# Performance work log

Measured on AMD Instinct MI355X. Metric: run time of the kernel, lower is better.

## Reference

```python
import jax, jax.numpy as jnp
import numpy as np

K = 20  # max object ids (ids 1..K); masks value 0 = background
EPS_GN = 1e-5

def _conv3(x, w, b):
    # 3x3 conv, padding=1 == SAME, NCHW/OIHW
    y = jax.lax.conv_general_dilated(x, w, (1, 1), 'SAME',
                                     dimension_numbers=('NCHW', 'OIHW', 'NCHW'))
    return y + b[None, :, None, None]

def _groupnorm(x, groups, w, b):
    B, C, H, W = x.shape
    xg = x.reshape(B, groups, C // groups, H, W)
    m = xg.mean(axis=(2, 3, 4), keepdims=True)
    v = xg.var(axis=(2, 3, 4), keepdims=True)
    xn = ((xg - m) * jax.lax.rsqrt(v + EPS_GN)).reshape(B, C, H, W)
    return xn * w[None, :, None, None] + b[None, :, None, None]


def setup_inputs() -> dict:
    key = jax.random.key(0)
    ks = jax.random.split(key, 8)
    def p(k, shape, s=0.05):
        return jax.random.normal(k, shape, jnp.float32) * s
    return {
        'x': jax.random.normal(ks[0], (4, 512, 128, 128), jnp.float32),
        'masks': jax.random.randint(ks[1], (4, 128, 128), 0, 21, jnp.int32),
        'w1': p(ks[2], (256, 512, 3, 3)), 'b1': jnp.zeros((256,), jnp.float32),
        'g1w': jnp.ones((256,), jnp.float32), 'g1b': jnp.zeros((256,), jnp.float32),
        'w2': p(ks[3], (128, 256, 3, 3)), 'b2': jnp.zeros((128,), jnp.float32),
        'g2w': jnp.ones((128,), jnp.float32), 'g2b': jnp.zeros((128,), jnp.float32),
        'w3': p(ks[4], (64, 128, 3, 3)), 'b3': jnp.zeros((64,), jnp.float32),
        'g3w': jnp.ones((64,), jnp.float32), 'g3b': jnp.zeros((64,), jnp.float32),
        'wb': p(ks[5], (7, 64)), 'bb': jnp.zeros((7,), jnp.float32),
        'wc': p(ks[6], (1, 64)), 'bc': jnp.zeros((1,), jnp.float32),
    }


def reference(x, masks, w1, b1, g1w, g1b, w2, b2, g2w, g2b,
              w3, b3, g3w, g3b, wb, bb, wc, bc):
    # encoder: (conv3 -> GN -> relu) x3
    h = jax.nn.relu(_groupnorm(_conv3(x, w1, b1), 8, g1w, g1b))
    h = jax.nn.relu(_groupnorm(_conv3(h, w2, b2), 4, g2w, g2b))
    h = jax.nn.relu(_groupnorm(_conv3(h, w3, b3), 4, g3w, g3b))  # [B,64,H,W]

    # masked segment-mean pooling over all ids 1..K (vectorized unique-loop)
    ids = jnp.arange(1, K + 1, dtype=masks.dtype)
    onehot = (masks[:, None, :, :] == ids[None, :, None, None]).astype(h.dtype)  # [B,K,H,W]
    sums = jnp.einsum('bchw,bkhw->bkc', h, onehot)          # [B,K,64]
    counts = onehot.sum(axis=(2, 3))                        # [B,K]
    pooled = sums / (counts[..., None] + 1e-6)              # [B,K,64]

    # 1x1 conv heads on pooled vector == dense matmuls
    boxes = jnp.einsum('bkc,oc->bko', pooled, wb) + bb      # [B,K,7]
    scores = jax.nn.sigmoid(jnp.einsum('bkc,oc->bko', pooled, wc) + bc)[..., 0]  # [B,K]
    return (boxes, scores)
```

## Files before the change

### kernel.cpp

```cpp
#include <hip/hip_runtime.h>
#include <hip/hip_bf16.h>
#include <math.h>

#define HW 16384
#define BATCH 4
#define KIDS 20

using short8 = __attribute__((ext_vector_type(8))) short;
using f32x4  = __attribute__((ext_vector_type(4))) float;

__device__ __forceinline__ unsigned short bfbits(float f) {
  __hip_bfloat16 h = __float2bfloat16(f);
  return *(unsigned short*)&h;
}

__device__ __forceinline__ void gload_lds16(const void* g, void* l) {
  __builtin_amdgcn_global_load_lds(
      (const __attribute__((address_space(1))) void*)g,
      (__attribute__((address_space(3))) void*)l, 16, 0, 0);
}

__global__ __launch_bounds__(256) void zero_k(float* __restrict__ p, int n) {
  int i = blockIdx.x*256 + threadIdx.x;
  if (i < n) p[i] = 0.f;
}

__global__ __launch_bounds__(256) void x_to_nhwc_k(const float* __restrict__ in,
                                                   __hip_bfloat16* __restrict__ out)
{
  __shared__ float tile[32][65];
  int t = blockIdx.x;
  const int pxt = t & 255; t >>= 8;
  const int ct  = t & 15;  t >>= 4;
  const int b   = t;
  const int tid = threadIdx.x;
  #pragma unroll
  for (int it = 0; it < 8; ++it) {
    int idx = tid + it*256;
    int px_l = idx & 63, c_l = idx >> 6;
    tile[c_l][px_l] = in[((size_t)(b*512 + ct*32 + c_l))*HW + pxt*64 + px_l];
  }
  __syncthreads();
  #pragma unroll
  for (int it = 0; it < 4; ++it) {
    int idx = tid + it*256;
    int c2 = idx & 15, px_l = idx >> 4;
    unsigned u = ((unsigned)bfbits(tile[c2*2+1][px_l]) << 16) | bfbits(tile[c2*2][px_l]);
    *(unsigned*)(out + ((size_t)(b*HW + pxt*64 + px_l))*512 + ct*32 + c2*2) = u;
  }
}

template<int Co, int Ci>
__global__ __launch_bounds__(256) void pack_w_k(const float* __restrict__ w,
                                                __hip_bfloat16* __restrict__ out)
{
  const int i = blockIdx.x*256 + threadIdx.x;
  const int ci = i & (Ci-1);
  const int r  = i >> __builtin_ctz(Ci);
  const int co = r & (Co-1);
  const int t  = r >> __builtin_ctz(Co);
  out[i] = __float2bfloat16(w[((size_t)co*Ci + ci)*9 + t]);
}

template<int Ci, int Co, int CPG, int MT>
__global__ __launch_bounds__(512, 2) void conv_mfma_k(
    const __hip_bfloat16* __restrict__ xin,
    const __hip_bfloat16* __restrict__ wpk,
    const float* __restrict__ bias,
    float* __restrict__ out,
    float* __restrict__ partS, float* __restrict__ partSS)
{
  constexpr int NT  = 4;
  constexpr int RG  = 64;
  constexpr int NC  = Ci/32;
  constexpr int NGW = (MT*16)/CPG;
  constexpr int WCO = 2*MT*16;
  constexpr int WSEG = WCO/16;
  constexpr int IBs = 4*10*512;
  constexpr int WLs = 9*WSEG*512;
  __shared__ __align__(16) short lds[2*IBs + WLs + 512];
  short* const wlds  = lds + 2*IBs;
  short* const trash = lds + 2*IBs + WLs;

  const int b  = blockIdx.x / RG;
  const int r0 = (blockIdx.x % RG) * 2;
  const int co0 = blockIdx.y * WCO;
  const int tid = threadIdx.x;
  const int wave = tid >> 6, lane = tid & 63;
  const int row_w = wave & 1;
  const int pw    = (wave >> 1) & 1;
  const int coh   = wave >> 2;
  const int co_w  = co0 + coh*MT*16;
  const int y = r0 + row_w;
  const int lr = lane & 15, q = lane >> 4;
  const int ls = lane & 15, lq = lane >> 4;

  {
    short8 z = {0,0,0,0,0,0,0,0};
    for (int i = tid; i < 1024; i += 512) {
      int u = i >> 6, m = i & 63;
      int buf = u >> 3, r = (u >> 1) & 3, side = u & 1;
      *((short8*)(lds + buf*IBs + r*5120 + side*9*512) + m) = z;
    }
    if (r0 == 0) {
      for (int i = tid; i < 2*640; i += 512) {
        int buf = i / 640, m = i % 640;
        *((short8*)(lds + buf*IBs + 0*5120) + m) = z;
      }
    }
    if (r0 == 126) {
      for (int i = tid; i < 2*640; i += 512) {
        int buf = i / 640, m = i % 640;
        *((short8*)(lds + buf*IBs + 3*5120) + m) = z;
      }
    }
  }

  const size_t in_base = (size_t)b * HW * Ci;

  auto stage_i = [&](int buf, int ci0) {
    #pragma unroll
    for (int it = 0; it < 4; ++it) {
      int gi = wave*4 + it;
      int r = gi >> 3, sd = (gi & 7) + 1;
      int yy = r0 + r - 1;
      bool ok = (unsigned)yy < 128u;
      int yc = ok ? yy : 0;
      const __hip_bfloat16* src = xin + in_base
          + (size_t)(yc*128 + (sd-1)*16 + ls)*Ci + ci0 + lq*8;
      short* dst = ok ? (lds + buf*IBs + r*5120 + sd*512) : trash;
      gload_lds16(src, dst);
    }
  };
  auto stage_w = [&](int ci0) {
    for (int u = wave; u < 9*WSEG; u += 8) {
      int t = u / WSEG, cs = u % WSEG;
      gload_lds16(wpk + ((size_t)(t*Co + co0 + cs*16 + ls))*Ci + ci0 + lq*8,
                  wlds + u*512);
    }
  };

  int base_dx[3];
  #pragma unroll
  for (int dx = 0; dx < 3; ++dx) {
    int e = dx + 15 + lr;
    base_dx[dx] = row_w*5120 + pw*2048 + (e>>4)*512 + (e&15)*8 + q*128;
  }
  const int base_a = coh*MT*512 + q*128 + lr*8;

  f32x4 acc[MT][NT] = {};
  stage_i(0, 0);
  __syncthreads();
  int cur = 0;
  for (int c = 0; c < NC; ++c) {
    const int ci0 = c*32;
    stage_w(ci0);
    if (c+1 < NC) {
      stage_i(cur^1, ci0 + 32);
      asm volatile("s_waitcnt vmcnt(4)" ::: "memory");
    } else {
      asm volatile("s_waitcnt vmcnt(0)" ::: "memory");
    }
    __builtin_amdgcn_s_barrier();
    __builtin_amdgcn_sched_barrier(0);
    const short* ib = lds + cur*IBs;

    short8 af[2][MT], bf[2][NT];
    #pragma unroll
    for (int mt = 0; mt < MT; ++mt)
      af[0][mt] = *(const short8*)(wlds + base_a + mt*512);
    #pragma unroll
    for (int nt = 0; nt < NT; ++nt)
      bf[0][nt] = *(const short8*)(ib + base_dx[0] + nt*512);

    #pragma unroll
    for (int t = 0; t < 9; ++t) {
      const int cb = t & 1, nb = cb ^ 1;
      if (t < 8) {
        const int t1 = t + 1, dy1 = t1/3, dx1 = t1%3;
        const short* wt = wlds + t1*WSEG*512;
        #pragma unroll
        for (int mt = 0; mt < MT; ++mt)
          af[nb][mt] = *(const short8*)(wt + base_a + mt*512);
        #pragma unroll
        for (int nt = 0; nt < NT; ++nt)
          bf[nb][nt] = *(const short8*)(ib + base_dx[dx1] + dy1*5120 + nt*512);
      }
      #pragma unroll
      for (int mt = 0; mt < MT; ++mt)
        #pragma unroll
        for (int nt = 0; nt < NT; ++nt)
          acc[mt][nt] = __builtin_amdgcn_mfma_f32_16x16x32_bf16(
              af[cb][mt], bf[cb][nt], acc[mt][nt], 0, 0, 0);
    }
    __builtin_amdgcn_s_barrier();
    cur ^= 1;
  }

  float sg[NGW] = {}, ssg[NGW] = {};
  #pragma unroll
  for (int mt = 0; mt < MT; ++mt) {
    const int g = (mt*16) / CPG;
    #pragma unroll
    for (int nt = 0; nt < NT; ++nt) {
      int px = pw*64 + nt*16 + lr;
      int co = co_w + mt*16 + q*4;
      const float4 bv = *(const float4*)(bias + co);
      f32x4 v = acc[mt][nt];
      v[0] += bv.x; v[1] += bv.y; v[2] += bv.z; v[3] += bv.w;
      sg[g]  += v[0] + v[1] + v[2] + v[3];
      ssg[g] += v[0]*v[0] + v[1]*v[1] + v[2]*v[2] + v[3]*v[3];
      *(f32x4*)(out + ((size_t)(b*HW + y*128 + px))*Co + co) = v;
    }
  }
  const int bgbase = b*(Co/CPG) + co_w/CPG;
  #pragma unroll
  for (int g = 0; g < NGW; ++g) {
    float s = sg[g], ss = ssg[g];
    #pragma unroll
    for (int off = 32; off; off >>= 1) {
      s  += __shfl_xor(s, off);
      ss += __shfl_xor(ss, off);
    }
    if (lane == 0) {
      atomicAdd(&partS[bgbase + g], s);
      atomicAdd(&partSS[bgbase + g], ss);
    }
  }
}

__global__ void gn_final_k(const float* __restrict__ partS,
                           const float* __restrict__ partSS,
                           float* __restrict__ mv, int nbg, float inv_n)
{
  const int i = threadIdx.x;
  if (i < nbg) {
    float s = partS[i], ss = partSS[i];
    float mean = s*inv_n, var = ss*inv_n - mean*mean;
    mv[2*i] = mean; mv[2*i+1] = rsqrtf(var + 1e-5f);
  }
}

template<int C, int CPG, bool BF16OUT>
__global__ __launch_bounds__(256) void gn_apply_k(const float* __restrict__ in,
    const float* __restrict__ mv, const float* __restrict__ gw,
    const float* __restrict__ gb, void* __restrict__ outp)
{
  constexpr int C4 = C/4;
  constexpr int G = C/CPG;
  const int i = blockIdx.x*256 + threadIdx.x;
  const int c4 = i & (C4-1);
  const int pxb = i >> __builtin_ctz(C4);
  const int b = pxb >> 14;
  const int c = c4*4;
  const int bg = b*G + c/CPG;
  const float mean = mv[2*bg], inv = mv[2*bg+1];
  float4 v = *((const float4*)in + i);
  const float4 w4 = *(const float4*)(gw + c);
  const float4 b4 = *(const float4*)(gb + c);
  float r0 = fmaxf((v.x-mean)*inv*w4.x + b4.x, 0.f);
  float r1 = fmaxf((v.y-mean)*inv*w4.y + b4.y, 0.f);
  float r2 = fmaxf((v.z-mean)*inv*w4.z + b4.z, 0.f);
  float r3 = fmaxf((v.w-mean)*inv*w4.w + b4.w, 0.f);
  if (BF16OUT) {
    uint2 o;
    o.x = ((unsigned)bfbits(r1) << 16) | bfbits(r0);
    o.y = ((unsigned)bfbits(r3) << 16) | bfbits(r2);
    *(uint2*)((__hip_bfloat16*)outp + (size_t)i*4) = o;
  } else {
    *((float4*)outp + i) = make_float4(r0,r1,r2,r3);
  }
}

__global__ __launch_bounds__(256) void pool_counts_k(
    const int* __restrict__ masks, float* __restrict__ counts)
{
  __shared__ int hist[KIDS];
  const int b = blockIdx.x;
  if (threadIdx.x < KIDS) hist[threadIdx.x] = 0;
  __syncthreads();
  for (int p = threadIdx.x; p < HW; p += 256) {
    const int m = masks[b*HW + p];
    if (m > 0) atomicAdd(&hist[m-1], 1);
  }
  __syncthreads();
  if (threadIdx.x < KIDS) counts[b*KIDS + threadIdx.x] = (float)hist[threadIdx.x];
}

__global__ __launch_bounds__(256) void pool_sums_k(const float* __restrict__ h3,
    const int* __restrict__ masks, float* __restrict__ sums)
{
  __shared__ float acc[KIDS*64];
  const int b = blockIdx.x >> 5, chunk = blockIdx.x & 31;
  const int tid = threadIdx.x;
  for (int j = tid; j < KIDS*64; j += 256) acc[j] = 0.f;
  __syncthreads();
  const int ch = tid & 63, pi = tid >> 6;
  const int p0 = chunk*512;
  for (int p = p0 + pi; p < p0 + 512; p += 4) {
    int m = masks[b*HW + p];
    if (m > 0) atomicAdd(&acc[(m-1)*64 + ch], h3[((size_t)(b*HW + p))*64 + ch]);
  }
  __syncthreads();
  for (int j = tid; j < KIDS*64; j += 256) atomicAdd(&sums[b*KIDS*64 + j], acc[j]);
}

__global__ __launch_bounds__(64) void heads_k(
    const float* __restrict__ sums, const float* __restrict__ counts,
    const float* __restrict__ wb, const float* __restrict__ bb,
    const float* __restrict__ wc, const float* __restrict__ bc,
    float* __restrict__ out)
{
  const int bk = blockIdx.x;
  const int c = threadIdx.x;
  const float pooled = sums[bk*64 + c] / (counts[bk] + 1e-6f);
  #pragma unroll
  for (int o = 0; o < 7; ++o) {
    float t = pooled * wb[o*64 + c];
    for (int off = 32; off > 0; off >>= 1) t += __shfl_down(t, off);
    if (c == 0) out[bk*7 + o] = t + bb[o];
  }
  float t = pooled * wc[c];
  for (int off = 32; off > 0; off >>= 1) t += __shfl_down(t, off);
  if (c == 0) out[BATCH*KIDS*7 + bk] = 1.f / (1.f + expf(-(t + bc[0])));
}

extern "C" void kernel_launch(void* const* d_in, const int* in_sizes, int n_in,
                              void* d_out, int out_size, void* d_ws, size_t ws_size,
                              hipStream_t stream)
{
  const float* x     = (const float*)d_in[0];
  const int*   masks = (const int*)  d_in[1];
  const float* w1 = (const float*)d_in[2];
  const float* b1 = (const float*)d_in[3];
  const float* g1w= (const float*)d_in[4];
  const float* g1b= (const float*)d_in[5];
  const float* w2 = (const float*)d_in[6];
  const float* b2 = (const float*)d_in[7];
  const float* g2w= (const float*)d_in[8];
  const float* g2b= (const float*)d_in[9];
  const float* w3 = (const float*)d_in[10];
  const float* b3 = (const float*)d_in[11];
  const float* g3w= (const float*)d_in[12];
  const float* g3b= (const float*)d_in[13];
  const float* wb = (const float*)d_in[14];
  const float* bb = (const float*)d_in[15];
  const float* wc = (const float*)d_in[16];
  const float* bc = (const float*)d_in[17];
  float* out = (float*)d_out;

  char* ws = (char*)d_ws;
  __hip_bfloat16* xb  = (__hip_bfloat16*)ws;
  __hip_bfloat16* h1b = (__hip_bfloat16*)ws;
  __hip_bfloat16* h2b = (__hip_bfloat16*)(ws + (size_t)(32<<20));
  float*          h3  = (float*)         (ws + (size_t)(48<<20));
  float* c1 = (float*)(ws + (size_t)(64<<20));
  float* c2 = c1;
  float* c3 = (float*)(ws + (size_t)(96<<20));
  __hip_bfloat16* wp1 = (__hip_bfloat16*)(ws + (size_t)(128<<20));
  __hip_bfloat16* wp2 = wp1 + 9*256*512;
  __hip_bfloat16* wp3 = wp2 + 9*128*256;
  char* tail = (char*)(wp3 + 9*64*128);
  float* mv     = (float*)tail;
  float* partS  = mv + 64;
  float* partSS = partS + 64;
  float* sums   = partSS + 64;
  float* counts = sums + 5120;

  zero_k<<<21, 256, 0, stream>>>(partS, 64 + 64 + 5120);

  x_to_nhwc_k<<<16384, 256, 0, stream>>>(x, xb);
  pack_w_k<256,512><<<4608, 256, 0, stream>>>(w1, wp1);
  pack_w_k<128,256><<<1152, 256, 0, stream>>>(w2, wp2);
  pack_w_k< 64,128><<< 288, 256, 0, stream>>>(w3, wp3);

  conv_mfma_k<512,256,32,4><<<dim3(256,2), 512, 0, stream>>>(
      xb, wp1, b1, c1, partS, partSS);
  gn_final_k<<<1, 64, 0, stream>>>(partS, partSS, mv, 32, 1.f/(32.f*HW));
  gn_apply_k<256,32,true><<<16384, 256, 0, stream>>>(c1, mv, g1w, g1b, h1b);

  conv_mfma_k<256,128,32,4><<<dim3(256,1), 512, 0, stream>>>(
      h1b, wp2, b2, c2, partS + 32, partSS + 32);
  gn_final_k<<<1, 64, 0, stream>>>(partS + 32, partSS + 32, mv, 16, 1.f/(32.f*HW));
  gn_apply_k<128,32,true><<<8192, 256, 0, stream>>>(c2, mv, g2w, g2b, h2b);

  conv_mfma_k<128,64,16,2><<<dim3(256,1), 512, 0, stream>>>(
      h2b, wp3, b3, c3, partS + 48, partSS + 48);
  gn_final_k<<<1, 64, 0, stream>>>(partS + 48, partSS + 48, mv, 16, 1.f/(16.f*HW));
  gn_apply_k<64,16,false><<<4096, 256, 0, stream>>>(c3, mv, g3w, g3b, h3);

  pool_counts_k<<<BATCH, 256, 0, stream>>>(masks, counts);
  pool_sums_k<<<BATCH*32, 256, 0, stream>>>(h3, masks, sums);
  heads_k<<<BATCH*KIDS, 64, 0, stream>>>(sums, counts, wb, bb, wc, bc, out);
}
```

Baseline: 747.8 us.

## Add wide-tile conv kernel for layer 1 and simplify fragment loading

Adds a new conv kernel for the first conv layer in which each block computes 4 rows by 128 pixels by 128 output channels, with 4x8 MFMA tiles per wave. Each staged input and weight tile therefore feeds more MFMAs, and the grid shrinks to 128x2 blocks. The new kernel uses a single LDS buffer with a sync per channel chunk instead of double buffering, so load and compute no longer overlap. The existing kernel also drops its register double-buffering of A/B fragments in favour of plain per-tap loads, which cuts register pressure at the risk of exposing LDS latency.

```diff
diff --git a/kernel.cpp b/kernel.cpp
--- a/kernel.cpp
+++ b/kernel.cpp
@@ -60,6 +60,140 @@
   const int co = r & (Co-1);
   const int t  = r >> __builtin_ctz(Co);
   out[i] = __float2bfloat16(w[((size_t)co*Ci + ci)*9 + t]);
+}
+
+template<int Ci, int Co, int CPG>
+__global__ __launch_bounds__(512, 2) void conv_wide_k(
+    const __hip_bfloat16* __restrict__ xin,
+    const __hip_bfloat16* __restrict__ wpk,
+    const float* __restrict__ bias,
+    float* __restrict__ out,
+    float* __restrict__ partS, float* __restrict__ partSS)
+{
+  constexpr int MT = 4, NT = 8;
+  constexpr int NC  = Ci/32;
+  constexpr int WCO = 128;
+  constexpr int NGW = 64/CPG;
+  constexpr int IBs = 6*10*512;
+  constexpr int WLs = 9*(WCO/16)*512;
+  __shared__ __align__(16) short lds[IBs + WLs + 512];
+  short* const wlds  = lds + IBs;
+  short* const trash = lds + IBs + WLs;
+
+  const int bx = blockIdx.x;
+  const int b  = bx >> 5;
+  const int r0 = (bx & 31) * 4;
+  const int co0 = blockIdx.y * WCO;
+  const int tid = threadIdx.x;
+  const int wave = tid >> 6, lane = tid & 63;
+  const int row_w = wave & 3;
+  const int coh   = wave >> 2;
+  const int y = r0 + row_w;
+  const int lr = lane & 15, q = lane >> 4;
+  const int ls = lane & 15, lq = lane >> 4;
+
+  {
+    short8 z = {0,0,0,0,0,0,0,0};
+    for (int i = tid; i < 12*64; i += 512) {
+      int u = i >> 6, m = i & 63;
+      int r = u >> 1, side = u & 1;
+      *((short8*)(lds + r*5120 + side*9*512) + m) = z;
+    }
+    if (r0 == 0)
+      for (int i = tid; i < 640; i += 512) *((short8*)lds + i) = z;
+    if (r0 == 124)
+      for (int i = tid; i < 640; i += 512) *((short8*)(lds + 5*5120) + i) = z;
+  }
+
+  const size_t in_base = (size_t)b * HW * Ci;
+
+  auto stage_i = [&](int ci0) {
+    #pragma unroll
+    for (int j = 0; j < 6; ++j) {
+      int u = wave*6 + j;
+      int r = u >> 3, seg = u & 7;
+      int yy = r0 + r - 1;
+      bool ok = (unsigned)yy < 128u;
+      const __hip_bfloat16* src = xin + in_base
+          + (size_t)((ok ? yy : 0)*128 + seg*16 + ls)*Ci + ci0 + lq*8;
+      short* dst = ok ? (lds + (r*10 + seg + 1)*512) : trash;
+      gload_lds16(src, dst);
+    }
+  };
+  auto stage_w = [&](int ci0) {
+    #pragma unroll
+    for (int j = 0; j < 9; ++j) {
+      gload_lds16(wpk + ((size_t)(j*Co + co0 + wave*16 + ls))*Ci + ci0 + lq*8,
+                  wlds + (j*8 + wave)*512);
+    }
+  };
+
+  int base_dx[3];
+  #pragma unroll
+  for (int dx = 0; dx < 3; ++dx) {
+    int e = dx + 15 + lr;
+    base_dx[dx] = row_w*5120 + (e>>4)*512 + (e&15)*8 + q*128;
+  }
+  const int base_a = coh*4*512 + q*128 + lr*8;
+
+  f32x4 acc[MT][NT] = {};
+  __syncthreads();
+  for (int c = 0; c < NC; ++c) {
+    const int ci0 = c*32;
+    stage_w(ci0);
+    stage_i(ci0);
+    __syncthreads();
+    #pragma unroll
+    for (int t = 0; t < 9; ++t) {
+      const int dy = t/3, dx = t%3;
+      short8 af[MT], bf[NT];
+      #pragma unroll
+      for (int mt = 0; mt < MT; ++mt)
+        af[mt] = *(const short8*)(wlds + t*4096 + base_a + mt*512);
+      #pragma unroll
+      for (int nt = 0; nt < NT; ++nt)
+        bf[nt] = *(const short8*)(lds + base_dx[dx] + dy*5120 + nt*512);
+      #pragma unroll
+      for (int mt = 0; mt < MT; ++mt)
+        #pragma unroll
+        for (int nt = 0; nt < NT; ++nt)
+          acc[mt][nt] = __builtin_amdgcn_mfma_f32_16x16x32_bf16(
+              af[mt], bf[nt], acc[mt][nt], 0, 0, 0);
+    }
+    __builtin_amdgcn_sched_barrier(0);
+    __builtin_amdgcn_s_barrier();
+  }
+
+  float sg[NGW] = {}, ssg[NGW] = {};
+  #pragma unroll
+  for (int mt = 0; mt < MT; ++mt) {
+    const int g = (mt*16) / CPG;
+    #pragma unroll
+    for (int nt = 0; nt < NT; ++nt) {
+      int px = nt*16 + lr;
+      int co = co0 + coh*64 + mt*16 + q*4;
+      const float4 bv = *(const float4*)(bias + co);
+      f32x4 v = acc[mt][nt];
+      v[0] += bv.x; v[1] += bv.y; v[2] += bv.z; v[3] += bv.w;
+      sg[g]  += v[0] + v[1] + v[2] + v[3];
+      ssg[g] += v[0]*v[0] + v[1]*v[1] + v[2]*v[2] + v[3]*v[3];
+      *(f32x4*)(out + ((size_t)(b*HW + y*128 + px))*Co + co) = v;
+    }
+  }
+  const int bgbase = b*(Co/CPG) + (co0 + coh*64)/CPG;
+  #pragma unroll
+  for (int g = 0; g < NGW; ++g) {
+    float s = sg[g], ss = ssg[g];
+    #pragma unroll
+    for (int off = 32; off; off >>= 1) {
+      s  += __shfl_xor(s, off);
+      ss += __shfl_xor(ss, off);
+    }
+    if (lane == 0) {
+      atomicAdd(&partS[bgbase + g], s);
+      atomicAdd(&partSS[bgbase + g], ss);
+    }
+  }
 }
 
 template<int Ci, int Co, int CPG, int MT>
@@ -105,7 +239,7 @@
     if (r0 == 0) {
       for (int i = tid; i < 2*640; i += 512) {
         int buf = i / 640, m = i % 640;
-        *((short8*)(lds + buf*IBs + 0*5120) + m) = z;
+        *((short8*)(lds + buf*IBs) + m) = z;
       }
     }
     if (r0 == 126) {
@@ -162,37 +296,25 @@
       asm volatile("s_waitcnt vmcnt(0)" ::: "memory");
     }
     __builtin_amdgcn_s_barrier();
-    __builtin_amdgcn_sched_barrier(0);
     const short* ib = lds + cur*IBs;
-
-    short8 af[2][MT], bf[2][NT];
-    #pragma unroll
-    for (int mt = 0; mt < MT; ++mt)
-      af[0][mt] = *(const short8*)(wlds + base_a + mt*512);
-    #pragma unroll
-    for (int nt = 0; nt < NT; ++nt)
-      bf[0][nt] = *(const short8*)(ib + base_dx[0] + nt*512);
-
     #pragma unroll
     for (int t = 0; t < 9; ++t) {
-      const int cb = t & 1, nb = cb ^ 1;
-      if (t < 8) {
-        const int t1 = t + 1, dy1 = t1/3, dx1 = t1%3;
-        const short* wt = wlds + t1*WSEG*512;
-        #pragma unroll
-        for (int mt = 0; mt < MT; ++mt)
-          af[nb][mt] = *(const short8*)(wt + base_a + mt*512);
-        #pragma unroll
-        for (int nt = 0; nt < NT; ++nt)
-          bf[nb][nt] = *(const short8*)(ib + base_dx[dx1] + dy1*5120 + nt*512);
-      }
+      const int dy = t/3, dx = t%3;
+      short8 af[MT], bf[NT];
+      #pragma unroll
+      for (int mt = 0; mt < MT; ++mt)
+        af[mt] = *(const short8*)(wlds + t*WSEG*512 + base_a + mt*512);
+      #pragma unroll
+      for (int nt = 0; nt < NT; ++nt)
+        bf[nt] = *(const short8*)(ib + base_dx[dx] + dy*5120 + nt*512);
       #pragma unroll
       for (int mt = 0; mt < MT; ++mt)
         #pragma unroll
         for (int nt = 0; nt < NT; ++nt)
           acc[mt][nt] = __builtin_amdgcn_mfma_f32_16x16x32_bf16(
-              af[cb][mt], bf[cb][nt], acc[mt][nt], 0, 0, 0);
-    }
+              af[mt], bf[nt], acc[mt][nt], 0, 0, 0);
+    }
+    __builtin_amdgcn_sched_barrier(0);
     __builtin_amdgcn_s_barrier();
     cur ^= 1;
   }
@@ -374,7 +496,7 @@
   pack_w_k<128,256><<<1152, 256, 0, stream>>>(w2, wp2);
   pack_w_k< 64,128><<< 288, 256, 0, stream>>>(w3, wp3);
 
-  conv_mfma_k<512,256,32,4><<<dim3(256,2), 512, 0, stream>>>(
+  conv_wide_k<512,256,32><<<dim3(128,2), 512, 0, stream>>>(
       xb, wp1, b1, c1, partS, partSS);
   gn_final_k<<<1, 64, 0, stream>>>(partS, partSS, mv, 32, 1.f/(32.f*HW));
   gn_apply_k<256,32,true><<<16384, 256, 0, stream>>>(c1, mv, g1w, g1b, h1b);
```

After: 697.6 us. -6.7%, faster.
